# Optimization experiments

Hardware: AMD Instinct MI355X
Metric: run time of the kernel (lower is better)

## Reference

```python
import jax, jax.numpy as jnp
import numpy as np

B, T, DK, DV, N = 4, 1024, 128, 128, 65536
TOPK = 32

def setup_inputs() -> dict:
    key = jax.random.key(0)
    k1, k2, k3 = jax.random.split(key, 3)
    q = jax.random.normal(k1, (B, T, DK), dtype=jnp.float32)
    keys = jax.random.normal(k2, (N, DK), dtype=jnp.float32)
    values = jax.random.normal(k3, (N, DV), dtype=jnp.float32)
    return {"q": q, "keys": keys, "values": values, "topk": TOPK}

def reference(q, keys, values, topk):
    # scores: [B, T, N] dense dot-product score matrix
    scores = jnp.einsum('btd,nd->btn', q, keys)
    k = min(topk, keys.shape[0])
    _, idx = jax.lax.top_k(scores, k)          # idx: [B, T, k]
    K_mem = keys[idx]                          # [B, T, k, Dk] gather
    V_mem = values[idx]                        # [B, T, k, Dv] gather
    return (K_mem, V_mem)
```

## Files before the change

### kernel.cpp

```cpp
#include <hip/hip_runtime.h>
#include <float.h>

#define NQ      4096
#define NKEYS   65536
#define DKDIM   128
#define DVDIM   128
#define TOPK_N  32
#define NSPLIT  16
#define KPS     (NKEYS / NSPLIT)
#define BQ      64
#define NCAND   (NSPLIT * TOPK_N)
#define NARROW  128
#define NOUT    ((size_t)NQ * TOPK_N * DKDIM)
#define KPT     32
#define NT      (KPS / KPT)

typedef __attribute__((ext_vector_type(8))) short short8;
typedef __attribute__((ext_vector_type(4))) float v4f;

__device__ inline unsigned short f2bf(float f) {
    unsigned int u = __float_as_uint(f);
    return (unsigned short)((u + 0x7FFFu + ((u >> 16) & 1u)) >> 16);
}

__device__ inline unsigned packpk(float s, unsigned li) {
    unsigned u = __float_as_uint(s);
    u = ((int)u < 0) ? ~u : (u | 0x80000000u);
    return (u & 0xFFFFF000u) | (4095u - li);
}
__device__ inline float unpack_lb(unsigned pk) {
    const unsigned m = pk & 0xFFFFF000u;
    const unsigned b = (m & 0x80000000u) ? (m & 0x7FFFFFFFu) : ~m;
    return __uint_as_float(b);
}

#define CEXU(p, s, desc) {                                                  \
    const unsigned _o = (unsigned)__shfl_xor((int)(p), (s));                \
    const bool _first = (p) > _o;                                           \
    const bool _keep  = (_first == (((l16 & (s)) == 0) == (desc)));         \
    (p) = _keep ? (p) : _o; }
#define CEXUI(pa, pb) { if ((pb) > (pa)) { const unsigned _t=(pa); (pa)=(pb); (pb)=_t; } }

__device__ __forceinline__ void sortmergeU(
    unsigned& p0, unsigned& p1, const int cc,
    const unsigned* __restrict__ bqr, const int l16)
{
    unsigned s0 = (l16      < cc) ? bqr[l16]      : 0u;
    unsigned s1 = (l16 + 16 < cc) ? bqr[l16 + 16] : 0u;

    CEXU(s0, 1, ((l16 & 2) == 0)); CEXU(s1, 1, ((l16 & 2) == 0));
    CEXU(s0, 2, ((l16 & 4) == 0)); CEXU(s1, 2, ((l16 & 4) == 0));
    CEXU(s0, 1, ((l16 & 4) == 0)); CEXU(s1, 1, ((l16 & 4) == 0));
    CEXU(s0, 4, ((l16 & 8) == 0)); CEXU(s1, 4, ((l16 & 8) == 0));
    CEXU(s0, 2, ((l16 & 8) == 0)); CEXU(s1, 2, ((l16 & 8) == 0));
    CEXU(s0, 1, ((l16 & 8) == 0)); CEXU(s1, 1, ((l16 & 8) == 0));
    CEXU(s0, 8, true);  CEXU(s1, 8, false);
    CEXU(s0, 4, true);  CEXU(s1, 4, false);
    CEXU(s0, 2, true);  CEXU(s1, 2, false);
    CEXU(s0, 1, true);  CEXU(s1, 1, false);
    CEXUI(s0, s1);
    CEXU(s0, 8, true);  CEXU(s1, 8, true);
    CEXU(s0, 4, true);  CEXU(s1, 4, true);
    CEXU(s0, 2, true);  CEXU(s1, 2, true);
    CEXU(s0, 1, true);  CEXU(s1, 1, true);

    unsigned c0 = (unsigned)__shfl_xor((int)s1, 15);
    unsigned c1 = (unsigned)__shfl_xor((int)s0, 15);

    CEXUI(p0, c0);
    CEXUI(p1, c1);
    CEXUI(p0, p1);
    CEXU(p0, 8, true); CEXU(p1, 8, true);
    CEXU(p0, 4, true); CEXU(p1, 4, true);
    CEXU(p0, 2, true); CEXU(p1, 2, true);
    CEXU(p0, 1, true); CEXU(p1, 1, true);
}

__global__ __launch_bounds__(256) void convert_kernel(
    const float* __restrict__ q, const float* __restrict__ keys,
    unsigned short* __restrict__ qbf, unsigned short* __restrict__ kbf)
{
    const size_t QG = (size_t)NQ * DKDIM / 8;
    const size_t KG = (size_t)NKEYS * DKDIM / 8;
    const size_t g  = (size_t)blockIdx.x * 256 + threadIdx.x;
    if (g >= QG + KG) return;
    const float* src;
    unsigned short* dst;
    if (g < QG) { src = q + g * 8;         dst = qbf + g * 8; }
    else        { const size_t h = g - QG; src = keys + h * 8; dst = kbf + h * 8; }
    const float4 a = ((const float4*)src)[0];
    const float4 b = ((const float4*)src)[1];
    short8 o;
    o[0] = (short)f2bf(a.x); o[1] = (short)f2bf(a.y);
    o[2] = (short)f2bf(a.z); o[3] = (short)f2bf(a.w);
    o[4] = (short)f2bf(b.x); o[5] = (short)f2bf(b.y);
    o[6] = (short)f2bf(b.z); o[7] = (short)f2bf(b.w);
    *(short8*)dst = o;
}

__global__ __launch_bounds__(256, 6) void score_select_kernel(
    const unsigned short* __restrict__ qbf, const unsigned short* __restrict__ kbf,
    unsigned* __restrict__ cand)
{
    __shared__ unsigned short kst[2][KPT * DKDIM];
    __shared__ unsigned bq[BQ][33];

    const int tid  = threadIdx.x;
    const int wave = tid >> 6;
    const int lane = tid & 63;
    const int l16  = lane & 15;
    const int quad = lane >> 4;

    const int lin   = blockIdx.y * gridDim.x + blockIdx.x;
    const int split = ((lin & 7) << 1) | (lin >> 9);
    const int qgrp  = (lin >> 3) & 63;
    const int q0    = qgrp * BQ + wave * 16;
    const int nbase = split * KPS;

    unsigned* __restrict__ bqr = &bq[wave * 16 + l16][0];

    short8 afrag[4];
#pragma unroll
    for (int t = 0; t < 4; ++t)
        afrag[t] = *(const short8*)(qbf + (size_t)(q0 + l16) * DKDIM + t * 32 + quad * 8);

    unsigned pk0[4], pk1[4];
#pragma unroll
    for (int r = 0; r < 4; ++r) { pk0[r] = 0u; pk1[r] = 0u; }
    float vmf = -FLT_MAX;
    int   cnt = 0;

    auto select32 = [&](const v4f a1, const v4f a2, const int n0loc) {
        const int h0 = a1[0] > vmf, h1 = a1[1] > vmf, h2 = a1[2] > vmf, h3 = a1[3] > vmf;
        const int h4 = a2[0] > vmf, h5 = a2[1] > vmf, h6 = a2[2] > vmf, h7 = a2[3] > vmf;
        const int nh = h0 + h1 + h2 + h3 + h4 + h5 + h6 + h7;
        const int s16   = __shfl_xor(nh, 16);
        const int psum  = nh + s16;
        const int sx32  = __shfl_xor(psum, 32);
        const int nhcol = psum + sx32;
        if (__ballot(cnt + nhcol > 32)) {
#pragma unroll
            for (int r = 0; r < 4; ++r) {
                const int cc = __shfl(cnt, quad * 4 + r);
                sortmergeU(pk0[r], pk1[r], cc, &bq[wave * 16 + quad * 4 + r][0], l16);
            }
            const unsigned t0 = (unsigned)__shfl((int)pk1[0], (l16 >> 2) * 16 + 15);
            const unsigned t1 = (unsigned)__shfl((int)pk1[1], (l16 >> 2) * 16 + 15);
            const unsigned t2 = (unsigned)__shfl((int)pk1[2], (l16 >> 2) * 16 + 15);
            const unsigned t3 = (unsigned)__shfl((int)pk1[3], (l16 >> 2) * 16 + 15);
            const unsigned a01 = (l16 & 1) ? t1 : t0;
            const unsigned a23 = (l16 & 1) ? t3 : t2;
            vmf = unpack_lb((l16 & 2) ? a23 : a01);
            cnt = 0;
        }
        int pos = cnt + ((quad & 1) ? s16 : 0) + ((quad & 2) ? sx32 : 0);
        const unsigned lb = (unsigned)(n0loc + quad * 4);
        if (h0) { bqr[pos] = packpk(a1[0], lb);      ++pos; }
        if (h1) { bqr[pos] = packpk(a1[1], lb + 1);  ++pos; }
        if (h2) { bqr[pos] = packpk(a1[2], lb + 2);  ++pos; }
        if (h3) { bqr[pos] = packpk(a1[3], lb + 3);  ++pos; }
        if (h4) { bqr[pos] = packpk(a2[0], lb + 16); ++pos; }
        if (h5) { bqr[pos] = packpk(a2[1], lb + 17); ++pos; }
        if (h6) { bqr[pos] = packpk(a2[2], lb + 18); ++pos; }
        if (h7) { bqr[pos] = packpk(a2[3], lb + 19); }
        cnt += nhcol;
    };

    const unsigned short* ksrc = kbf + (size_t)nbase * DKDIM;
    const int c0 = tid, c1 = tid + 256;
    const int d0 = ((c0 >> 4) * 128) + (((c0 & 15) ^ ((c0 >> 4) & 7)) * 8);
    const int d1 = ((c1 >> 4) * 128) + (((c1 & 15) ^ ((c1 >> 4) & 7)) * 8);

    {
        const short8 a = *(const short8*)(ksrc + c0 * 8);
        const short8 b = *(const short8*)(ksrc + c1 * 8);
        *(short8*)&kst[0][d0] = a;
        *(short8*)&kst[0][d1] = b;
    }
    __syncthreads();

    int cur = 0;
    const int sx = l16 & 7;
    for (int t = 0; t < NT; ++t) {
        short8 nA, nB;
        const bool more = (t + 1 < NT);
        if (more) {
            const unsigned short* s = ksrc + (size_t)(t + 1) * (KPT * DKDIM);
            nA = *(const short8*)(s + c0 * 8);
            nB = *(const short8*)(s + c1 * 8);
        }
        const unsigned short* kr0 = &kst[cur][(l16) * 128];
        const unsigned short* kr1 = &kst[cur][(16 + l16) * 128];
        v4f acc1 = {0.f, 0.f, 0.f, 0.f};
        v4f acc2 = {0.f, 0.f, 0.f, 0.f};
#pragma unroll
        for (int tt = 0; tt < 4; ++tt) {
            const short8 b0 = *(const short8*)(kr0 + ((quad + tt * 4) ^ sx) * 8);
            const short8 b1 = *(const short8*)(kr1 + ((quad + tt * 4) ^ sx) * 8);
            acc1 = __builtin_amdgcn_mfma_f32_16x16x32_bf16(b0, afrag[tt], acc1, 0, 0, 0);
            acc2 = __builtin_amdgcn_mfma_f32_16x16x32_bf16(b1, afrag[tt], acc2, 0, 0, 0);
        }
        select32(acc1, acc2, t * KPT);
        if (more) {
            *(short8*)&kst[cur ^ 1][d0] = nA;
            *(short8*)&kst[cur ^ 1][d1] = nB;
        }
        __syncthreads();
        cur ^= 1;
    }

#pragma unroll
    for (int r = 0; r < 4; ++r) {
        const int cc = __shfl(cnt, quad * 4 + r);
        sortmergeU(pk0[r], pk1[r], cc, &bq[wave * 16 + quad * 4 + r][0], l16);
        const size_t base = ((size_t)(q0 + quad * 4 + r) * NSPLIT + split) * TOPK_N;
        cand[base + l16]      = pk0[r];
        cand[base + 16 + l16] = pk1[r];
    }
}

__global__ __launch_bounds__(512) void rescore_gather_kernel(
    const float* __restrict__ qg, const float* __restrict__ keys,
    const float* __restrict__ values, const unsigned* __restrict__ cand,
    float* __restrict__ out)
{
    __shared__ float    qrow[DKDIM];
    __shared__ unsigned spk[NCAND];
    __shared__ int      sn[NCAND];
    __shared__ float    ss[NARROW];
    __shared__ int      si[NARROW];
    const int bt  = blockIdx.x;
    const int tid = threadIdx.x;

    if (tid < DKDIM) qrow[tid] = qg[(size_t)bt * DKDIM + tid];
    {
        const unsigned pk = cand[(size_t)bt * NCAND + tid];
        spk[tid] = pk;
        sn[tid]  = (tid >> 5) * KPS + (int)(4095u - (pk & 0xFFFu));
    }
    __syncthreads();

    for (int k = 2; k <= NCAND; k <<= 1) {
        for (int j = k >> 1; j > 0; j >>= 1) {
            const int ixj = tid ^ j;
            if (ixj > tid) {
                const bool dirDesc = ((tid & k) == 0);
                const unsigned pa = spk[tid], pb = spk[ixj];
                const int      na = sn[tid],  nb = sn[ixj];
                const bool before = (pa > pb) || (pa == pb && na < nb);
                if (before != dirDesc) {
                    spk[tid] = pb; spk[ixj] = pa;
                    sn[tid]  = nb; sn[ixj]  = na;
                }
            }
            __syncthreads();
        }
    }

    if (tid < NARROW) {
        const int n = sn[tid];
        const float4* krow = (const float4*)(keys + (size_t)n * DKDIM);
        float s = 0.f;
#pragma unroll
        for (int d4 = 0; d4 < DKDIM / 4; ++d4) {
            const float4 k4 = krow[d4];
            const float4 q4 = *(const float4*)&qrow[4 * d4];
            s = fmaf(q4.x, k4.x, s);
            s = fmaf(q4.y, k4.y, s);
            s = fmaf(q4.z, k4.z, s);
            s = fmaf(q4.w, k4.w, s);
        }
        ss[tid] = s; si[tid] = n;
    }
    __syncthreads();

    for (int k = 2; k <= NARROW; k <<= 1) {
        for (int j = k >> 1; j > 0; j >>= 1) {
            const int ixj = tid ^ j;
            if (tid < NARROW && ixj > tid) {
                const bool dirDesc = ((tid & k) == 0);
                const float sa = ss[tid], sb = ss[ixj];
                const int   ia = si[tid], ib = si[ixj];
                const bool before = (sa > sb) || (sa == sb && ia < ib);
                if (before != dirDesc) {
                    ss[tid] = sb; ss[ixj] = sa;
                    si[tid] = ib; si[ixj] = ia;
                }
            }
            __syncthreads();
        }
    }

    const int lane = tid & 31;
    const int rb   = tid >> 5;
#pragma unroll
    for (int r = 0; r < 2; ++r) {
        const int row = rb + 16 * r;
        const int n   = si[row];
        const float4 kv = *(const float4*)(keys   + (size_t)n * DKDIM + 4 * lane);
        const float4 vv = *(const float4*)(values + (size_t)n * DVDIM + 4 * lane);
        const size_t ob = ((size_t)bt * TOPK_N + row) * DKDIM + 4 * lane;
        *(float4*)(out + ob)        = kv;
        *(float4*)(out + NOUT + ob) = vv;
    }
}

extern "C" void kernel_launch(void* const* d_in, const int* in_sizes, int n_in,
                              void* d_out, int out_size, void* d_ws, size_t ws_size,
                              hipStream_t stream)
{
    const float* q      = (const float*)d_in[0];
    const float* keys   = (const float*)d_in[1];
    const float* values = (const float*)d_in[2];
    float* out = (float*)d_out;

    unsigned short* qbf = (unsigned short*)d_ws;
    unsigned short* kbf = (unsigned short*)((char*)d_ws + (1u << 20));
    unsigned* cand = (unsigned*)((char*)d_ws + (17u << 20));

    const int cvt_groups = (NQ + NKEYS) * DKDIM / 8;
    convert_kernel<<<(cvt_groups + 255) / 256, 256, 0, stream>>>(q, keys, qbf, kbf);
    score_select_kernel<<<dim3(NQ / BQ, NSPLIT), 256, 0, stream>>>(qbf, kbf, cand);
    rescore_gather_kernel<<<NQ, 512, 0, stream>>>(q, keys, values, cand, out);
}
```

Measured before the change: 602.3 us.

## Double key splits and single-buffer key tile to raise occupancy

The key set is split into 32 chunks instead of 16, so the scoring grid has twice as many blocks, each scanning half as many keys. The shared-memory key tile goes from double to single buffering, with an extra barrier per step, so more blocks fit per CU (launch bounds raised to 8). The rescore kernel now loops over twice as many candidates per query and runs a longer bitonic sort, which adds sort and load work to the second stage in exchange for more parallelism in the first.

Measured after the change: 865.0 us. 1.44x slower.

```diff
diff --git a/kernel.cpp b/kernel.cpp
--- a/kernel.cpp
+++ b/kernel.cpp
@@ -6,7 +6,7 @@
 #define DKDIM   128
 #define DVDIM   128
 #define TOPK_N  32
-#define NSPLIT  16
+#define NSPLIT  32
 #define KPS     (NKEYS / NSPLIT)
 #define BQ      64
 #define NCAND   (NSPLIT * TOPK_N)
@@ -98,11 +98,11 @@
     *(short8*)dst = o;
 }
 
-__global__ __launch_bounds__(256, 6) void score_select_kernel(
+__global__ __launch_bounds__(256, 8) void score_select_kernel(
     const unsigned short* __restrict__ qbf, const unsigned short* __restrict__ kbf,
     unsigned* __restrict__ cand)
 {
-    __shared__ unsigned short kst[2][KPT * DKDIM];
+    __shared__ unsigned short kst[KPT * DKDIM];
     __shared__ unsigned bq[BQ][33];
 
     const int tid  = threadIdx.x;
@@ -112,8 +112,9 @@
     const int quad = lane >> 4;
 
     const int lin   = blockIdx.y * gridDim.x + blockIdx.x;
-    const int split = ((lin & 7) << 1) | (lin >> 9);
-    const int qgrp  = (lin >> 3) & 63;
+    const int rest  = lin >> 3;
+    const int split = ((lin & 7) << 2) | (rest & 3);
+    const int qgrp  = rest >> 2;
     const int q0    = qgrp * BQ + wave * 16;
     const int nbase = split * KPS;
 
@@ -174,12 +175,11 @@
     {
         const short8 a = *(const short8*)(ksrc + c0 * 8);
         const short8 b = *(const short8*)(ksrc + c1 * 8);
-        *(short8*)&kst[0][d0] = a;
-        *(short8*)&kst[0][d1] = b;
+        *(short8*)&kst[d0] = a;
+        *(short8*)&kst[d1] = b;
     }
     __syncthreads();
 
-    int cur = 0;
     const int sx = l16 & 7;
     for (int t = 0; t < NT; ++t) {
         short8 nA, nB;
@@ -189,8 +189,8 @@
             nA = *(const short8*)(s + c0 * 8);
             nB = *(const short8*)(s + c1 * 8);
         }
-        const unsigned short* kr0 = &kst[cur][(l16) * 128];
-        const unsigned short* kr1 = &kst[cur][(16 + l16) * 128];
+        const unsigned short* kr0 = &kst[(l16) * 128];
+        const unsigned short* kr1 = &kst[(16 + l16) * 128];
         v4f acc1 = {0.f, 0.f, 0.f, 0.f};
         v4f acc2 = {0.f, 0.f, 0.f, 0.f};
 #pragma unroll
@@ -201,12 +201,12 @@
             acc2 = __builtin_amdgcn_mfma_f32_16x16x32_bf16(b1, afrag[tt], acc2, 0, 0, 0);
         }
         select32(acc1, acc2, t * KPT);
+        __syncthreads();
         if (more) {
-            *(short8*)&kst[cur ^ 1][d0] = nA;
-            *(short8*)&kst[cur ^ 1][d1] = nB;
-        }
-        __syncthreads();
-        cur ^= 1;
+            *(short8*)&kst[d0] = nA;
+            *(short8*)&kst[d1] = nB;
+            __syncthreads();
+        }
     }
 
 #pragma unroll
@@ -233,24 +233,28 @@
     const int tid = threadIdx.x;
 
     if (tid < DKDIM) qrow[tid] = qg[(size_t)bt * DKDIM + tid];
-    {
-        const unsigned pk = cand[(size_t)bt * NCAND + tid];
-        spk[tid] = pk;
-        sn[tid]  = (tid >> 5) * KPS + (int)(4095u - (pk & 0xFFFu));
+#pragma unroll
+    for (int e = tid; e < NCAND; e += 512) {
+        const unsigned pk = cand[(size_t)bt * NCAND + e];
+        spk[e] = pk;
+        sn[e]  = (e >> 5) * KPS + (int)(4095u - (pk & 0xFFFu));
     }
     __syncthreads();
 
     for (int k = 2; k <= NCAND; k <<= 1) {
         for (int j = k >> 1; j > 0; j >>= 1) {
-            const int ixj = tid ^ j;
-            if (ixj > tid) {
-                const bool dirDesc = ((tid & k) == 0);
-                const unsigned pa = spk[tid], pb = spk[ixj];
-                const int      na = sn[tid],  nb = sn[ixj];
-                const bool before = (pa > pb) || (pa == pb && na < nb);
-                if (before != dirDesc) {
-                    spk[tid] = pb; spk[ixj] = pa;
-                    sn[tid]  = nb; sn[ixj]  = na;
+#pragma unroll
+            for (int e = tid; e < NCAND; e += 512) {
+                const int ixj = e ^ j;
+                if (ixj > e) {
+                    const bool dirDesc = ((e & k) == 0);
+                    const unsigned pa = spk[e], pb = spk[ixj];
+                    const int      na = sn[e],  nb = sn[ixj];
+                    const bool before = (pa > pb) || (pa == pb && na < nb);
+                    if (before != dirDesc) {
+                        spk[e] = pb; spk[ixj] = pa;
+                        sn[e]  = nb; sn[ixj]  = na;
+                    }
                 }
             }
             __syncthreads();
```
